# Optimization experiments

Hardware: AMD Instinct MI355X
Metric: run time of the kernel (lower is better)

Reference implementation:

```python
import jax, jax.numpy as jnp
import numpy as np

B, N, H, W = 8, 16384, 64, 64
CTX, OUT, ST = 32, 2, 1
HID = [516, 256, 128, 64, 32, 16]
IN_SIZE = CTX + 2 + ST + OUT  # 37


def _bilinear_sample(img, coord):
    """torch F.grid_sample, mode=bilinear, padding=zeros, align_corners=False.
    img: [B,C,H,W]; coord: [B,N,2] (x,y in [-1,1]). Returns [B,C,N]."""
    _, _, Hh, Ww = img.shape
    gx = (coord[..., 0] + 1.0) * (Ww * 0.5) - 0.5
    gy = (coord[..., 1] + 1.0) * (Hh * 0.5) - 0.5
    x0 = jnp.floor(gx)
    y0 = jnp.floor(gy)
    wx1 = gx - x0
    wy1 = gy - y0

    def tap(xi, yi, w):
        valid = (xi >= 0) & (xi < Ww) & (yi >= 0) & (yi < Hh)
        xc = jnp.clip(xi, 0, Ww - 1).astype(jnp.int32)
        yc = jnp.clip(yi, 0, Hh - 1).astype(jnp.int32)
        vals = jax.vmap(lambda im, y, x: im[:, y, x])(img, yc, xc)  # [B,C,N]
        return vals * (w * valid)[:, None, :]

    return (tap(x0, y0, (1 - wx1) * (1 - wy1))
            + tap(x0 + 1, y0, wx1 * (1 - wy1))
            + tap(x0, y0 + 1, (1 - wx1) * wy1)
            + tap(x0 + 1, y0 + 1, wx1 * wy1))


def _layer_shapes():
    shapes = [(IN_SIZE, HID[0])]
    for i in range(len(HID) - 1):
        shapes.append((HID[i] + IN_SIZE, HID[i + 1]))
    shapes.append((HID[-1], OUT))
    return shapes


def setup_inputs():
    key = jax.random.key(0)
    ks = jax.random.split(key, 4 + 7)
    inp = {
        "lr_fields": jax.random.normal(ks[0], (B, OUT, H, W), jnp.float32),
        "context_grid": jax.random.normal(ks[1], (B, CTX, H, W), jnp.float32),
        "hr_eps": jax.random.normal(ks[2], (B, H, W), jnp.float32),
        "coord": jax.random.uniform(ks[3], (B, N, 2), jnp.float32, -1.0, 1.0),
    }
    for j, (fi, fo) in enumerate(_layer_shapes()):
        inp[f"W{j}"] = jax.random.normal(ks[4 + j], (fi, fo), jnp.float32) / np.sqrt(fi)
        inp[f"b{j}"] = jnp.zeros((fo,), jnp.float32)
    return inp


def reference(lr_fields, context_grid, hr_eps, coord,
              W0, b0, W1, b1, W2, b2, W3, b3, W4, b4, W5, b5, W6, b6):
    # original permutes (0,1,3,2) before grid_sample -> swap spatial axes
    ctx_pts = _bilinear_sample(jnp.swapaxes(context_grid, 2, 3), coord)  # [B,CTX,N]
    lr_pts = _bilinear_sample(jnp.swapaxes(lr_fields, 2, 3), coord)      # [B,OUT,N]
    eps_pts = _bilinear_sample(jnp.swapaxes(hr_eps[:, None], 2, 3), coord)  # [B,1,N]
    x_in = jnp.concatenate([
        jnp.transpose(ctx_pts, (0, 2, 1)),
        coord,
        jnp.transpose(lr_pts, (0, 2, 1)),
        jnp.transpose(eps_pts, (0, 2, 1)),
    ], axis=2)  # [B,N,37]
    x = jax.nn.relu(x_in @ W0 + b0)
    for Wl, bl in ((W1, b1), (W2, b2), (W3, b3), (W4, b4), (W5, b5)):
        x = jax.nn.relu(jnp.concatenate([x, x_in], axis=2) @ Wl + bl)
    return x @ W6 + b6  # [B,N,2]
```

## Files before the change

kernel.cpp:

```cpp
#include <hip/hip_runtime.h>


#define NTH     1024
#define NWAVES  16
#define MPTS    32
#define MTILES  (MPTS / 16)
#define SROW    872
#define XIN_OFF 0
#define HA_OFF  64
#define HB_OFF  608
#define NPOINTS (8 * 16384)
#define GRIDX   (NPOINTS / MPTS)
#define LDSBYTES (MPTS * SROW * 2)

#define SGB __builtin_amdgcn_sched_group_barrier
#define SG_MFMA   0x008
#define SG_VMREAD 0x020
#define SG_DSREAD 0x100

typedef short          short8  __attribute__((ext_vector_type(8)));
typedef short          short4v __attribute__((ext_vector_type(4)));
typedef float          f32x4   __attribute__((ext_vector_type(4)));
typedef unsigned short u16;

__device__ __forceinline__ u16 f2bf(float f) {
    unsigned int u = __builtin_bit_cast(unsigned int, f);
    u += 0x7fffu + ((u >> 16) & 1u);
    return (u16)(u >> 16);
}

__constant__ int pk_base8[8] = {0, 4224, 23680, 28800, 30336, 30848, 31040, 31104};
__constant__ int pk_ks[7]    = {2, 19, 10, 6, 4, 3, 1};
__constant__ int pk_khp[7]   = {0, 544, 256, 128, 64, 32, 32};
__constant__ int pk_kact[7]  = {0, 516, 256, 128, 64, 32, 16};
__constant__ int pk_nact[7]  = {516, 256, 128, 64, 32, 16, 2};

struct WPtrs { const float* W[7]; };

__global__ void pack_weights(WPtrs wp, u16* __restrict__ out)
{
    const int f = blockIdx.x * blockDim.x + threadIdx.x;
    if (f >= 31104) return;
    int l = 0;
    while (l < 6 && f >= pk_base8[l + 1]) ++l;
    const int r    = f - pk_base8[l];
    const int lane = r & 63;
    const int t    = r >> 6;
    const int ks   = pk_ks[l];
    const int s    = t % ks;
    const int nt   = t / ks;
    const int n    = nt * 16 + (lane & 15);
    const int k0   = s * 32 + (lane >> 4) * 8;
    const int nact = pk_nact[l];
    const int khp  = pk_khp[l];
    const int kact = pk_kact[l];
    const float* W = wp.W[l];

    union { short8 v; u16 e[8]; } frag;
#pragma unroll
    for (int j = 0; j < 8; ++j) {
        const int k = k0 + j;
        float v = 0.0f;
        if (n < nact) {
            if (k < khp) {
                if (k < kact) v = W[k * nact + n];
            } else {
                const int xr = k - khp;
                if (xr < 37) v = W[(kact + xr) * nact + n];
            }
        }
        frag.e[j] = f2bf(v);
    }
    *(short8*)(out + (size_t)f * 8) = frag.v;
}

template<int KHP, int HSEG, int OSEG, int NT, int NACT, int LBASE,
         bool XIN, bool RELU, bool GOUT>
__device__ __forceinline__ void mlayer(const u16* __restrict__ wpack,
                                       const float* __restrict__ bias,
                                       u16* __restrict__ s_act,
                                       float* __restrict__ gout, int p0,
                                       int wave, int lane)
{
    constexpr int KHS = KHP / 32;
    constexpr int KS  = KHS + (XIN ? 2 : 0);
    constexpr int MS  = MTILES;
    const int lm = lane & 15;
    const int lq = lane >> 4;
    const u16* wl = wpack + LBASE + lane * 8;

    const u16* arow[MS];
#pragma unroll
    for (int m = 0; m < MS; ++m)
        arow[m] = s_act + (m * 16 + lm) * SROW + lq * 8;

    for (int nt = wave; nt < NT; nt += NWAVES) {
        const u16* bp = wl + (size_t)nt * KS * 512;

        f32x4 acc[MS];
#pragma unroll
        for (int m = 0; m < MS; ++m)
            acc[m] = (f32x4){0.f, 0.f, 0.f, 0.f};

#pragma unroll
        for (int s = 0; s < KS; ++s) {
            const int ab = (s < KHS) ? (HSEG + s * 32)
                                     : (XIN_OFF + (s - KHS) * 32);
            short8 a[MS];
#pragma unroll
            for (int m = 0; m < MS; ++m)
                a[m] = *(const short8*)(arow[m] + ab);
            const short8 b = *(const short8*)(bp + (size_t)s * 512);
#pragma unroll
            for (int m = 0; m < MS; ++m)
                acc[m] = __builtin_amdgcn_mfma_f32_16x16x32_bf16(b, a[m], acc[m], 0, 0, 0);
        }

        SGB(SG_DSREAD, 2, 0); SGB(SG_VMREAD, 1, 0);
        if (KS > 1) { SGB(SG_DSREAD, 2, 0); SGB(SG_VMREAD, 1, 0); }
#pragma unroll
        for (int s = 0; s < KS; ++s) {
            SGB(SG_MFMA, 2, 0);
            if (s + 2 < KS) { SGB(SG_DSREAD, 2, 0); SGB(SG_VMREAD, 1, 0); }
        }

        const int bn = nt * 16 + lq * 4;
        float bv[4];
        if (bn + 4 <= NACT) {
            const f32x4 b4 = *(const f32x4*)(bias + bn);
            bv[0] = b4[0]; bv[1] = b4[1]; bv[2] = b4[2]; bv[3] = b4[3];
        } else {
#pragma unroll
            for (int r = 0; r < 4; ++r)
                bv[r] = (bn + r < NACT) ? bias[bn + r] : 0.f;
        }
        if (GOUT) {
            if (lq == 0) {
#pragma unroll
                for (int m = 0; m < MS; ++m) {
                    float2 o;
                    o.x = acc[m][0] + bv[0];
                    o.y = acc[m][1] + bv[1];
                    *(float2*)(gout + (size_t)(p0 + m * 16 + lm) * 2) = o;
                }
            }
        } else {
#pragma unroll
            for (int m = 0; m < MS; ++m) {
                short4v o;
#pragma unroll
                for (int r = 0; r < 4; ++r) {
                    float v = acc[m][r] + bv[r];
                    if (RELU) v = fmaxf(v, 0.f);
                    o[r] = (short)f2bf(v);
                }
                *(short4v*)(s_act + (size_t)(m * 16 + lm) * SROW + OSEG + bn) = o;
            }
        }
    }
}

struct MainParams {
    const float* lr;
    const float* ctx;
    const float* eps;
    const float* coord;
    const float* Bb[7];
    const u16*   wpack;
    float*       out;
};

__global__ __launch_bounds__(NTH, 8)
void cont_decoder_mfma(MainParams p)
{
    extern __shared__ u16 s_act[];
    __shared__ int   s_x0[MPTS], s_y0[MPTS];
    __shared__ float s_wx[MPTS], s_wy[MPTS];

    const int tid  = threadIdx.x;
    const int wave = tid >> 6;
    const int lane = tid & 63;
    const int p0   = blockIdx.x * MPTS;
    const int b    = p0 >> 14;

    for (int i = tid; i < MPTS * 43; i += NTH) {
        const int pt = i / 43, c = i % 43;
        const int col = (c < 27) ? (37 + c) : (592 + (c - 27));
        s_act[pt * SROW + col] = 0;
    }

    if (tid < MPTS) {
        const int pt = p0 + tid;
        const float cx = p.coord[2 * pt];
        const float cy = p.coord[2 * pt + 1];
        const float gx = (cx + 1.0f) * 32.0f - 0.5f;
        const float gy = (cy + 1.0f) * 32.0f - 0.5f;
        const float fx0 = floorf(gx), fy0 = floorf(gy);
        s_x0[tid] = (int)fx0;
        s_y0[tid] = (int)fy0;
        s_wx[tid] = gx - fx0;
        s_wy[tid] = gy - fy0;
        s_act[tid * SROW + 32] = f2bf(cx);
        s_act[tid * SROW + 33] = f2bf(cy);
    }
    __syncthreads();

    for (int idx = tid; idx < MPTS * 35; idx += NTH) {
        const int t = idx / 35;
        const int c = idx % 35;
        const float* base;
        int col;
        if (c < 32)      { base = p.ctx + (size_t)(b * 32 + c) * 4096;       col = c; }
        else if (c < 34) { base = p.lr  + (size_t)(b * 2 + (c - 32)) * 4096; col = 34 + (c - 32); }
        else             { base = p.eps + (size_t)b * 4096;                   col = 36; }

        const int   x0 = s_x0[t], y0 = s_y0[t];
        const float wx = s_wx[t], wy = s_wy[t];
        const int x1 = x0 + 1, y1 = y0 + 1;
        const bool xv0 = (x0 >= 0) & (x0 < 64);
        const bool xv1 = (x1 >= 0) & (x1 < 64);
        const bool yv0 = (y0 >= 0) & (y0 < 64);
        const bool yv1 = (y1 >= 0) & (y1 < 64);
        const int xc0 = min(max(x0, 0), 63), xc1 = min(max(x1, 0), 63);
        const int yc0 = min(max(y0, 0), 63), yc1 = min(max(y1, 0), 63);

        const float w00 = (1.0f - wx) * (1.0f - wy) * ((xv0 && yv0) ? 1.0f : 0.0f);
        const float w10 = wx * (1.0f - wy)          * ((xv1 && yv0) ? 1.0f : 0.0f);
        const float w01 = (1.0f - wx) * wy          * ((xv0 && yv1) ? 1.0f : 0.0f);
        const float w11 = wx * wy                   * ((xv1 && yv1) ? 1.0f : 0.0f);

        const float val = w00 * base[xc0 * 64 + yc0]
                        + w10 * base[xc1 * 64 + yc0]
                        + w01 * base[xc0 * 64 + yc1]
                        + w11 * base[xc1 * 64 + yc1];
        s_act[t * SROW + col] = f2bf(val);
    }
    __syncthreads();

    mlayer<  0,  HA_OFF, HA_OFF, 33, 516, 0,      true,  true,  false>(p.wpack, p.Bb[0], s_act, nullptr, p0, wave, lane);
    __syncthreads();
    mlayer<544,  HA_OFF, HB_OFF, 16, 256, 33792,  true,  true,  false>(p.wpack, p.Bb[1], s_act, nullptr, p0, wave, lane);
    __syncthreads();
    mlayer<256,  HB_OFF, HA_OFF,  8, 128, 189440, true,  true,  false>(p.wpack, p.Bb[2], s_act, nullptr, p0, wave, lane);
    __syncthreads();
    mlayer<128,  HA_OFF, HB_OFF,  4,  64, 230400, true,  true,  false>(p.wpack, p.Bb[3], s_act, nullptr, p0, wave, lane);
    __syncthreads();
    mlayer< 64,  HB_OFF, HA_OFF,  2,  32, 242688, true,  true,  false>(p.wpack, p.Bb[4], s_act, nullptr, p0, wave, lane);
    __syncthreads();
    mlayer< 32,  HA_OFF, HB_OFF,  1,  16, 246784, true,  true,  false>(p.wpack, p.Bb[5], s_act, nullptr, p0, wave, lane);
    __syncthreads();
    mlayer< 32,  HB_OFF, 0,       1,   2, 248320, false, false, true >(p.wpack, p.Bb[6], s_act, p.out,   p0, wave, lane);
}

extern "C" void kernel_launch(void* const* d_in, const int* in_sizes, int n_in,
                              void* d_out, int out_size, void* d_ws, size_t ws_size,
                              hipStream_t stream)
{
    WPtrs wp;
    for (int l = 0; l < 7; ++l) wp.W[l] = (const float*)d_in[4 + 2 * l];

    MainParams p;
    p.lr    = (const float*)d_in[0];
    p.ctx   = (const float*)d_in[1];
    p.eps   = (const float*)d_in[2];
    p.coord = (const float*)d_in[3];
    for (int l = 0; l < 7; ++l) p.Bb[l] = (const float*)d_in[5 + 2 * l];
    p.wpack = (const u16*)d_ws;
    p.out   = (float*)d_out;

    hipFuncSetAttribute((const void*)cont_decoder_mfma,
                        hipFuncAttributeMaxDynamicSharedMemorySize, LDSBYTES);

    hipLaunchKernelGGL(pack_weights, dim3(122), dim3(256), 0, stream, wp, (u16*)d_ws);
    hipLaunchKernelGGL(cont_decoder_mfma, dim3(GRIDX), dim3(NTH), LDSBYTES, stream, p);
}
```

Measured before the change: 220.8 us.

## Hand-pipeline MFMA operand loads with inline asm rings and explicit waitcnts

Replaces compiler-scheduled LDS and global operand loads in the MLP layer loop with inline-asm ds_read_b128 and global_load_dwordx4 issued into small ring buffers. Activations are prefetched three k-steps ahead and weights two ahead, with explicit s_waitcnt counters before each MFMA step. The goal is to overlap load latency with MFMA work more predictably than the sched_group_barrier hints did. In exchange it adds register pressure under 1024-thread launch bounds. The hand-counted waitcnts are fragile, since any compiler-generated memory operation in between would break the counts.

```diff
diff --git a/kernel.cpp b/kernel.cpp
--- a/kernel.cpp
+++ b/kernel.cpp
@@ -13,11 +13,6 @@
 #define GRIDX   (NPOINTS / MPTS)
 #define LDSBYTES (MPTS * SROW * 2)
 
-#define SGB __builtin_amdgcn_sched_group_barrier
-#define SG_MFMA   0x008
-#define SG_VMREAD 0x020
-#define SG_DSREAD 0x100
-
 typedef short          short8  __attribute__((ext_vector_type(8)));
 typedef short          short4v __attribute__((ext_vector_type(4)));
 typedef float          f32x4   __attribute__((ext_vector_type(4)));
@@ -28,6 +23,28 @@
     u += 0x7fffu + ((u >> 16) & 1u);
     return (u16)(u >> 16);
 }
+
+__device__ __forceinline__ unsigned lds_off(const void* p) {
+    return (unsigned)(unsigned long long)
+        (__attribute__((address_space(3))) const void*)p;
+}
+
+__device__ __forceinline__ short8 dsread128(unsigned addr) {
+    short8 d;
+    asm volatile("ds_read_b128 %0, %1" : "=v"(d) : "v"(addr));
+    return d;
+}
+__device__ __forceinline__ short8 gload128(const void* p) {
+    short8 d;
+    asm volatile("global_load_dwordx4 %0, %1, off" : "=v"(d) : "v"(p));
+    return d;
+}
+
+__device__ __forceinline__ void wvm0(){ asm volatile("s_waitcnt vmcnt(0)"   ::: "memory"); }
+__device__ __forceinline__ void wvm1(){ asm volatile("s_waitcnt vmcnt(1)"   ::: "memory"); }
+__device__ __forceinline__ void wlg0(){ asm volatile("s_waitcnt lgkmcnt(0)" ::: "memory"); }
+__device__ __forceinline__ void wlg2(){ asm volatile("s_waitcnt lgkmcnt(2)" ::: "memory"); }
+__device__ __forceinline__ void wlg4(){ asm volatile("s_waitcnt lgkmcnt(4)" ::: "memory"); }
 
 __constant__ int pk_base8[8] = {0, 4224, 23680, 28800, 30336, 30848, 31040, 31104};
 __constant__ int pk_ks[7]    = {2, 19, 10, 6, 4, 3, 1};
@@ -84,15 +101,19 @@
 {
     constexpr int KHS = KHP / 32;
     constexpr int KS  = KHS + (XIN ? 2 : 0);
+    constexpr int DA  = (KS < 3) ? KS : 3;
+    constexpr int DW  = (KS < 2) ? KS : 2;
     constexpr int MS  = MTILES;
     const int lm = lane & 15;
     const int lq = lane >> 4;
     const u16* wl = wpack + LBASE + lane * 8;
 
-    const u16* arow[MS];
+#define ABOFF(s_) (((s_) < KHS) ? (HSEG + (s_) * 32) : (XIN_OFF + ((s_) - KHS) * 32))
+
+    unsigned abase[MS];
 #pragma unroll
     for (int m = 0; m < MS; ++m)
-        arow[m] = s_act + (m * 16 + lm) * SROW + lq * 8;
+        abase[m] = lds_off(s_act + ((m * 16 + lm) * SROW + lq * 8));
 
     for (int nt = wave; nt < NT; nt += NWAVES) {
         const u16* bp = wl + (size_t)nt * KS * 512;
@@ -102,26 +123,37 @@
         for (int m = 0; m < MS; ++m)
             acc[m] = (f32x4){0.f, 0.f, 0.f, 0.f};
 
+        wlg0(); wvm0();
+
+        short8 wring[DW];
+#pragma unroll
+        for (int d = 0; d < DW; ++d)
+            wring[d] = gload128(bp + (size_t)d * 512);
+        short8 aring[DA][MS];
+#pragma unroll
+        for (int d = 0; d < DA; ++d)
+#pragma unroll
+            for (int m = 0; m < MS; ++m)
+                aring[d][m] = dsread128(abase[m] + 2u * ABOFF(d));
+
 #pragma unroll
         for (int s = 0; s < KS; ++s) {
-            const int ab = (s < KHS) ? (HSEG + s * 32)
-                                     : (XIN_OFF + (s - KHS) * 32);
-            short8 a[MS];
+            const int wv = ((KS - s) < DW ? (KS - s) : DW) - 1;
+            if (wv >= 1) wvm1(); else wvm0();
+            const int la = ((KS - s) < DA ? (KS - s) : DA) - 1;
+            if (la >= 2) wlg4(); else if (la == 1) wlg2(); else wlg0();
+            __builtin_amdgcn_sched_barrier(0);
 #pragma unroll
             for (int m = 0; m < MS; ++m)
-                a[m] = *(const short8*)(arow[m] + ab);
-            const short8 b = *(const short8*)(bp + (size_t)s * 512);
-#pragma unroll
-            for (int m = 0; m < MS; ++m)
-                acc[m] = __builtin_amdgcn_mfma_f32_16x16x32_bf16(b, a[m], acc[m], 0, 0, 0);
-        }
-
-        SGB(SG_DSREAD, 2, 0); SGB(SG_VMREAD, 1, 0);
-        if (KS > 1) { SGB(SG_DSREAD, 2, 0); SGB(SG_VMREAD, 1, 0); }
-#pragma unroll
-        for (int s = 0; s < KS; ++s) {
-            SGB(SG_MFMA, 2, 0);
-            if (s + 2 < KS) { SGB(SG_DSREAD, 2, 0); SGB(SG_VMREAD, 1, 0); }
+                acc[m] = __builtin_amdgcn_mfma_f32_16x16x32_bf16(
+                             wring[s % DW], aring[s % DA][m], acc[m], 0, 0, 0);
+            if (s + DW < KS)
+                wring[s % DW] = gload128(bp + (size_t)(s + DW) * 512);
+            if (s + DA < KS) {
+#pragma unroll
+                for (int m = 0; m < MS; ++m)
+                    aring[s % DA][m] = dsread128(abase[m] + 2u * ABOFF(s + DA));
+            }
         }
 
         const int bn = nt * 16 + lq * 4;
@@ -158,6 +190,7 @@
             }
         }
     }
+#undef ABOFF
 }
 
 struct MainParams {
```

Result: no change. 218.4 us (-1.1%).

## Double points per block and compute hidden layers in place with one LDS buffer

Applied to the files above, without the earlier changes.

Doubles the points handled per block from 32 to 64, so each weight fragment loaded from global memory feeds twice as many MFMAs. Replaces the two ping-pong activation buffers with a single in-place hidden segment: each wave keeps its accumulators in registers across a barrier, then overwrites the shared buffer, shrinking the row stride. This trades less global weight traffic for more registers per wave and an extra barrier per layer, and it drops the manual sched_group_barrier instruction interleaving. The first layer still loops over 33 column tiles, but writing them in place is safe because its only inputs are the x_in columns.

```diff
diff --git a/kernel.cpp b/kernel.cpp
--- a/kernel.cpp
+++ b/kernel.cpp
@@ -3,20 +3,14 @@
 
 #define NTH     1024
 #define NWAVES  16
-#define MPTS    32
+#define MPTS    64
 #define MTILES  (MPTS / 16)
-#define SROW    872
+#define SROW    616
 #define XIN_OFF 0
-#define HA_OFF  64
-#define HB_OFF  608
+#define HSEG    64
 #define NPOINTS (8 * 16384)
 #define GRIDX   (NPOINTS / MPTS)
 #define LDSBYTES (MPTS * SROW * 2)
-
-#define SGB __builtin_amdgcn_sched_group_barrier
-#define SG_MFMA   0x008
-#define SG_VMREAD 0x020
-#define SG_DSREAD 0x100
 
 typedef short          short8  __attribute__((ext_vector_type(8)));
 typedef short          short4v __attribute__((ext_vector_type(4)));
@@ -74,89 +68,54 @@
     *(short8*)(out + (size_t)f * 8) = frag.v;
 }
 
-template<int KHP, int HSEG, int OSEG, int NT, int NACT, int LBASE,
-         bool XIN, bool RELU, bool GOUT>
-__device__ __forceinline__ void mlayer(const u16* __restrict__ wpack,
-                                       const float* __restrict__ bias,
-                                       u16* __restrict__ s_act,
-                                       float* __restrict__ gout, int p0,
-                                       int wave, int lane)
+template<int KHP, bool XIN, int MS>
+__device__ __forceinline__ void unit_compute(const u16* __restrict__ bp,
+                                             const u16* const* arow,
+                                             f32x4* acc)
 {
     constexpr int KHS = KHP / 32;
     constexpr int KS  = KHS + (XIN ? 2 : 0);
-    constexpr int MS  = MTILES;
-    const int lm = lane & 15;
-    const int lq = lane >> 4;
-    const u16* wl = wpack + LBASE + lane * 8;
-
-    const u16* arow[MS];
-#pragma unroll
-    for (int m = 0; m < MS; ++m)
-        arow[m] = s_act + (m * 16 + lm) * SROW + lq * 8;
-
-    for (int nt = wave; nt < NT; nt += NWAVES) {
-        const u16* bp = wl + (size_t)nt * KS * 512;
-
-        f32x4 acc[MS];
+#pragma unroll
+    for (int s = 0; s < KS; ++s) {
+        const int ab = (s < KHS) ? (HSEG + s * 32)
+                                 : (XIN_OFF + (s - KHS) * 32);
+        short8 a[MS];
 #pragma unroll
         for (int m = 0; m < MS; ++m)
-            acc[m] = (f32x4){0.f, 0.f, 0.f, 0.f};
-
-#pragma unroll
-        for (int s = 0; s < KS; ++s) {
-            const int ab = (s < KHS) ? (HSEG + s * 32)
-                                     : (XIN_OFF + (s - KHS) * 32);
-            short8 a[MS];
-#pragma unroll
-            for (int m = 0; m < MS; ++m)
-                a[m] = *(const short8*)(arow[m] + ab);
-            const short8 b = *(const short8*)(bp + (size_t)s * 512);
-#pragma unroll
-            for (int m = 0; m < MS; ++m)
-                acc[m] = __builtin_amdgcn_mfma_f32_16x16x32_bf16(b, a[m], acc[m], 0, 0, 0);
-        }
-
-        SGB(SG_DSREAD, 2, 0); SGB(SG_VMREAD, 1, 0);
-        if (KS > 1) { SGB(SG_DSREAD, 2, 0); SGB(SG_VMREAD, 1, 0); }
-#pragma unroll
-        for (int s = 0; s < KS; ++s) {
-            SGB(SG_MFMA, 2, 0);
-            if (s + 2 < KS) { SGB(SG_DSREAD, 2, 0); SGB(SG_VMREAD, 1, 0); }
-        }
-
-        const int bn = nt * 16 + lq * 4;
-        float bv[4];
-        if (bn + 4 <= NACT) {
-            const f32x4 b4 = *(const f32x4*)(bias + bn);
-            bv[0] = b4[0]; bv[1] = b4[1]; bv[2] = b4[2]; bv[3] = b4[3];
-        } else {
-#pragma unroll
-            for (int r = 0; r < 4; ++r)
-                bv[r] = (bn + r < NACT) ? bias[bn + r] : 0.f;
-        }
-        if (GOUT) {
-            if (lq == 0) {
-#pragma unroll
-                for (int m = 0; m < MS; ++m) {
-                    float2 o;
-                    o.x = acc[m][0] + bv[0];
-                    o.y = acc[m][1] + bv[1];
-                    *(float2*)(gout + (size_t)(p0 + m * 16 + lm) * 2) = o;
-                }
-            }
-        } else {
-#pragma unroll
-            for (int m = 0; m < MS; ++m) {
-                short4v o;
-#pragma unroll
-                for (int r = 0; r < 4; ++r) {
-                    float v = acc[m][r] + bv[r];
-                    if (RELU) v = fmaxf(v, 0.f);
-                    o[r] = (short)f2bf(v);
-                }
-                *(short4v*)(s_act + (size_t)(m * 16 + lm) * SROW + OSEG + bn) = o;
-            }
-        }
+            a[m] = *(const short8*)(arow[m] + ab);
+        const short8 b = *(const short8*)(bp + (size_t)s * 512);
+#pragma unroll
+        for (int m = 0; m < MS; ++m)
+            acc[m] = __builtin_amdgcn_mfma_f32_16x16x32_bf16(b, a[m], acc[m], 0, 0, 0);
+    }
+}
+
+template<int NACT, bool RELU, int MS>
+__device__ __forceinline__ void unit_store_lds(const f32x4* acc,
+                                               const float* __restrict__ bias,
+                                               u16* __restrict__ s_act,
+                                               int nt, int lm, int lq)
+{
+    const int bn = nt * 16 + lq * 4;
+    float bv[4];
+    if (bn + 4 <= NACT) {
+        const f32x4 b4 = *(const f32x4*)(bias + bn);
+        bv[0] = b4[0]; bv[1] = b4[1]; bv[2] = b4[2]; bv[3] = b4[3];
+    } else {
+#pragma unroll
+        for (int r = 0; r < 4; ++r)
+            bv[r] = (bn + r < NACT) ? bias[bn + r] : 0.f;
+    }
+#pragma unroll
+    for (int m = 0; m < MS; ++m) {
+        short4v o;
+#pragma unroll
+        for (int r = 0; r < 4; ++r) {
+            float v = acc[m][r] + bv[r];
+            if (RELU) v = fmaxf(v, 0.f);
+            o[r] = (short)f2bf(v);
+        }
+        *(short4v*)(s_act + (size_t)(m * 16 + lm) * SROW + HSEG + bn) = o;
     }
 }
 
@@ -170,6 +129,30 @@
     float*       out;
 };
 
+template<int KHP, int NT, int NACT, int LBASE>
+__device__ __forceinline__ void mlayer_ip(const u16* __restrict__ wpack,
+                                          const float* __restrict__ bias,
+                                          u16* __restrict__ s_act,
+                                          const u16* const* arow,
+                                          int wave, int lane)
+{
+    constexpr int MS = MTILES;
+    const int lm = lane & 15;
+    const int lq = lane >> 4;
+    f32x4 acc[MS];
+#pragma unroll
+    for (int m = 0; m < MS; ++m) acc[m] = (f32x4){0.f, 0.f, 0.f, 0.f};
+
+    const bool active = (wave < NT);
+    if (active) {
+        const u16* bp = wpack + LBASE + lane * 8 + (size_t)wave * (KHP / 32 + 2) * 512;
+        unit_compute<KHP, true, MS>(bp, arow, acc);
+    }
+    __syncthreads();
+    if (active)
+        unit_store_lds<NACT, true, MS>(acc, bias, s_act, wave, lm, lq);
+}
+
 __global__ __launch_bounds__(NTH, 8)
 void cont_decoder_mfma(MainParams p)
 {
@@ -180,6 +163,8 @@
     const int tid  = threadIdx.x;
     const int wave = tid >> 6;
     const int lane = tid & 63;
+    const int lm   = lane & 15;
+    const int lq   = lane >> 4;
     const int p0   = blockIdx.x * MPTS;
     const int b    = p0 >> 14;
 
@@ -237,19 +222,51 @@
     }
     __syncthreads();
 
-    mlayer<  0,  HA_OFF, HA_OFF, 33, 516, 0,      true,  true,  false>(p.wpack, p.Bb[0], s_act, nullptr, p0, wave, lane);
-    __syncthreads();
-    mlayer<544,  HA_OFF, HB_OFF, 16, 256, 33792,  true,  true,  false>(p.wpack, p.Bb[1], s_act, nullptr, p0, wave, lane);
-    __syncthreads();
-    mlayer<256,  HB_OFF, HA_OFF,  8, 128, 189440, true,  true,  false>(p.wpack, p.Bb[2], s_act, nullptr, p0, wave, lane);
-    __syncthreads();
-    mlayer<128,  HA_OFF, HB_OFF,  4,  64, 230400, true,  true,  false>(p.wpack, p.Bb[3], s_act, nullptr, p0, wave, lane);
-    __syncthreads();
-    mlayer< 64,  HB_OFF, HA_OFF,  2,  32, 242688, true,  true,  false>(p.wpack, p.Bb[4], s_act, nullptr, p0, wave, lane);
-    __syncthreads();
-    mlayer< 32,  HA_OFF, HB_OFF,  1,  16, 246784, true,  true,  false>(p.wpack, p.Bb[5], s_act, nullptr, p0, wave, lane);
-    __syncthreads();
-    mlayer< 32,  HB_OFF, 0,       1,   2, 248320, false, false, true >(p.wpack, p.Bb[6], s_act, p.out,   p0, wave, lane);
+    const u16* arow[MTILES];
+#pragma unroll
+    for (int m = 0; m < MTILES; ++m)
+        arow[m] = s_act + (m * 16 + lm) * SROW + lq * 8;
+
+    {
+        for (int nt = wave; nt < 33; nt += NWAVES) {
+            f32x4 acc[MTILES];
+#pragma unroll
+            for (int m = 0; m < MTILES; ++m) acc[m] = (f32x4){0.f, 0.f, 0.f, 0.f};
+            const u16* bp = p.wpack + 0 + lane * 8 + (size_t)nt * 2 * 512;
+            unit_compute<0, true, MTILES>(bp, arow, acc);
+            unit_store_lds<516, true, MTILES>(acc, p.Bb[0], s_act, nt, lm, lq);
+        }
+    }
+    __syncthreads();
+
+    mlayer_ip<544, 16, 256, 33792 >(p.wpack, p.Bb[1], s_act, arow, wave, lane);
+    __syncthreads();
+    mlayer_ip<256,  8, 128, 189440>(p.wpack, p.Bb[2], s_act, arow, wave, lane);
+    __syncthreads();
+    mlayer_ip<128,  4,  64, 230400>(p.wpack, p.Bb[3], s_act, arow, wave, lane);
+    __syncthreads();
+    mlayer_ip< 64,  2,  32, 242688>(p.wpack, p.Bb[4], s_act, arow, wave, lane);
+    __syncthreads();
+    mlayer_ip< 32,  1,  16, 246784>(p.wpack, p.Bb[5], s_act, arow, wave, lane);
+    __syncthreads();
+
+    if (wave == 0) {
+        f32x4 acc[MTILES];
+#pragma unroll
+        for (int m = 0; m < MTILES; ++m) acc[m] = (f32x4){0.f, 0.f, 0.f, 0.f};
+        const u16* bp = p.wpack + 248320 + lane * 8;
+        unit_compute<32, false, MTILES>(bp, arow, acc);
+        if (lq == 0) {
+            const float b0 = p.Bb[6][0], b1 = p.Bb[6][1];
+#pragma unroll
+            for (int m = 0; m < MTILES; ++m) {
+                float2 o;
+                o.x = acc[m][0] + b0;
+                o.y = acc[m][1] + b1;
+                *(float2*)(p.out + (size_t)(p0 + m * 16 + lm) * 2) = o;
+            }
+        }
+    }
 }
 
 extern "C" void kernel_launch(void* const* d_in, const int* in_sizes, int n_in,
```

After: 222.2 us. No clear change (+0.6%).

## Double points per block, 2x8 wave grid, in-place activations with barrier

Applied to the files above, without the earlier changes.

Raises points per block from 32 to 64 and splits the 16 waves into 2 M-groups by 8 N-groups, each wave computing a 2x2 block of MFMA tiles so every loaded weight fragment is reused across more points. Activation ping-pong buffers are merged into one in-place hidden segment, with an internal __syncthreads between the compute and store phases for layers that read and write the same region. This shrinks the LDS row stride and halves grid size and per-point weight traffic, at the cost of more LDS per block, fewer blocks, and removal of the explicit scheduling barriers. Layer 0 reads only the input region, so it writes in place without the extra barrier.

```diff
diff --git a/kernel.cpp b/kernel.cpp
--- a/kernel.cpp
+++ b/kernel.cpp
@@ -3,20 +3,14 @@
 
 #define NTH     1024
 #define NWAVES  16
-#define MPTS    32
+#define MPTS    64
 #define MTILES  (MPTS / 16)
-#define SROW    872
+#define SROW    616
 #define XIN_OFF 0
-#define HA_OFF  64
-#define HB_OFF  608
+#define HSEG    64
 #define NPOINTS (8 * 16384)
 #define GRIDX   (NPOINTS / MPTS)
 #define LDSBYTES (MPTS * SROW * 2)
-
-#define SGB __builtin_amdgcn_sched_group_barrier
-#define SG_MFMA   0x008
-#define SG_VMREAD 0x020
-#define SG_DSREAD 0x100
 
 typedef short          short8  __attribute__((ext_vector_type(8)));
 typedef short          short4v __attribute__((ext_vector_type(4)));
@@ -74,92 +68,6 @@
     *(short8*)(out + (size_t)f * 8) = frag.v;
 }
 
-template<int KHP, int HSEG, int OSEG, int NT, int NACT, int LBASE,
-         bool XIN, bool RELU, bool GOUT>
-__device__ __forceinline__ void mlayer(const u16* __restrict__ wpack,
-                                       const float* __restrict__ bias,
-                                       u16* __restrict__ s_act,
-                                       float* __restrict__ gout, int p0,
-                                       int wave, int lane)
-{
-    constexpr int KHS = KHP / 32;
-    constexpr int KS  = KHS + (XIN ? 2 : 0);
-    constexpr int MS  = MTILES;
-    const int lm = lane & 15;
-    const int lq = lane >> 4;
-    const u16* wl = wpack + LBASE + lane * 8;
-
-    const u16* arow[MS];
-#pragma unroll
-    for (int m = 0; m < MS; ++m)
-        arow[m] = s_act + (m * 16 + lm) * SROW + lq * 8;
-
-    for (int nt = wave; nt < NT; nt += NWAVES) {
-        const u16* bp = wl + (size_t)nt * KS * 512;
-
-        f32x4 acc[MS];
-#pragma unroll
-        for (int m = 0; m < MS; ++m)
-            acc[m] = (f32x4){0.f, 0.f, 0.f, 0.f};
-
-#pragma unroll
-        for (int s = 0; s < KS; ++s) {
-            const int ab = (s < KHS) ? (HSEG + s * 32)
-                                     : (XIN_OFF + (s - KHS) * 32);
-            short8 a[MS];
-#pragma unroll
-            for (int m = 0; m < MS; ++m)
-                a[m] = *(const short8*)(arow[m] + ab);
-            const short8 b = *(const short8*)(bp + (size_t)s * 512);
-#pragma unroll
-            for (int m = 0; m < MS; ++m)
-                acc[m] = __builtin_amdgcn_mfma_f32_16x16x32_bf16(b, a[m], acc[m], 0, 0, 0);
-        }
-
-        SGB(SG_DSREAD, 2, 0); SGB(SG_VMREAD, 1, 0);
-        if (KS > 1) { SGB(SG_DSREAD, 2, 0); SGB(SG_VMREAD, 1, 0); }
-#pragma unroll
-        for (int s = 0; s < KS; ++s) {
-            SGB(SG_MFMA, 2, 0);
-            if (s + 2 < KS) { SGB(SG_DSREAD, 2, 0); SGB(SG_VMREAD, 1, 0); }
-        }
-
-        const int bn = nt * 16 + lq * 4;
-        float bv[4];
-        if (bn + 4 <= NACT) {
-            const f32x4 b4 = *(const f32x4*)(bias + bn);
-            bv[0] = b4[0]; bv[1] = b4[1]; bv[2] = b4[2]; bv[3] = b4[3];
-        } else {
-#pragma unroll
-            for (int r = 0; r < 4; ++r)
-                bv[r] = (bn + r < NACT) ? bias[bn + r] : 0.f;
-        }
-        if (GOUT) {
-            if (lq == 0) {
-#pragma unroll
-                for (int m = 0; m < MS; ++m) {
-                    float2 o;
-                    o.x = acc[m][0] + bv[0];
-                    o.y = acc[m][1] + bv[1];
-                    *(float2*)(gout + (size_t)(p0 + m * 16 + lm) * 2) = o;
-                }
-            }
-        } else {
-#pragma unroll
-            for (int m = 0; m < MS; ++m) {
-                short4v o;
-#pragma unroll
-                for (int r = 0; r < 4; ++r) {
-                    float v = acc[m][r] + bv[r];
-                    if (RELU) v = fmaxf(v, 0.f);
-                    o[r] = (short)f2bf(v);
-                }
-                *(short4v*)(s_act + (size_t)(m * 16 + lm) * SROW + OSEG + bn) = o;
-            }
-        }
-    }
-}
-
 struct MainParams {
     const float* lr;
     const float* ctx;
@@ -169,6 +77,140 @@
     const u16*   wpack;
     float*       out;
 };
+
+template<int NACT, bool RELU>
+__device__ __forceinline__ void store_nt(const f32x4* accm,
+                                         const float* __restrict__ bias,
+                                         u16* __restrict__ s_act,
+                                         int nt, int mbase, int lm, int lq)
+{
+    const int bn = nt * 16 + lq * 4;
+    float bv[4];
+    if (bn + 4 <= NACT) {
+        const f32x4 b4 = *(const f32x4*)(bias + bn);
+        bv[0] = b4[0]; bv[1] = b4[1]; bv[2] = b4[2]; bv[3] = b4[3];
+    } else {
+#pragma unroll
+        for (int r = 0; r < 4; ++r)
+            bv[r] = (bn + r < NACT) ? bias[bn + r] : 0.f;
+    }
+#pragma unroll
+    for (int m = 0; m < 2; ++m) {
+        short4v o;
+#pragma unroll
+        for (int r = 0; r < 4; ++r) {
+            float v = accm[m][r] + bv[r];
+            if (RELU) v = fmaxf(v, 0.f);
+            o[r] = (short)f2bf(v);
+        }
+        *(short4v*)(s_act + (size_t)((mbase + m) * 16 + lm) * SROW + HSEG + bn) = o;
+    }
+}
+
+template<int KHP, int NT, int NACT, int LBASE,
+         bool XIN, bool RELU, bool GOUT, bool IPBAR>
+__device__ __forceinline__ void mlayer(const u16* __restrict__ wpack,
+                                       const float* __restrict__ bias,
+                                       u16* __restrict__ s_act,
+                                       float* __restrict__ gout, int p0,
+                                       int wave, int lane)
+{
+    constexpr int KHS = KHP / 32;
+    constexpr int KS  = KHS + (XIN ? 2 : 0);
+    const int lm = lane & 15;
+    const int lq = lane >> 4;
+    const int mg = wave & 1;
+    const int ng = wave >> 1;
+    const int mbase = mg * 2;
+
+    const u16* arow0 = s_act + (size_t)((mbase * 16) + lm) * SROW + lq * 8;
+    const u16* arow1 = arow0 + (size_t)16 * SROW;
+    const u16* wl = wpack + LBASE + lane * 8;
+
+#define ABOFF(s_) (((s_) < KHS) ? (HSEG + (s_) * 32) : (XIN_OFF + ((s_) - KHS) * 32))
+
+    if constexpr (IPBAR) {
+        const int nt0 = ng, nt1 = ng + 8;
+        const bool act0 = nt0 < NT;
+        const bool act1 = nt1 < NT;
+        f32x4 acc[2][2];
+#pragma unroll
+        for (int i = 0; i < 2; ++i)
+#pragma unroll
+            for (int m = 0; m < 2; ++m)
+                acc[i][m] = (f32x4){0.f, 0.f, 0.f, 0.f};
+
+        if (act0) {
+            const u16* bp0 = wl + (size_t)nt0 * KS * 512;
+            const u16* bp1 = wl + (size_t)nt1 * KS * 512;
+#pragma unroll
+            for (int s = 0; s < KS; ++s) {
+                const int ab = ABOFF(s);
+                const short8 a0 = *(const short8*)(arow0 + ab);
+                const short8 a1 = *(const short8*)(arow1 + ab);
+                const short8 w0 = *(const short8*)(bp0 + (size_t)s * 512);
+                acc[0][0] = __builtin_amdgcn_mfma_f32_16x16x32_bf16(w0, a0, acc[0][0], 0, 0, 0);
+                acc[0][1] = __builtin_amdgcn_mfma_f32_16x16x32_bf16(w0, a1, acc[0][1], 0, 0, 0);
+                if (act1) {
+                    const short8 w1 = *(const short8*)(bp1 + (size_t)s * 512);
+                    acc[1][0] = __builtin_amdgcn_mfma_f32_16x16x32_bf16(w1, a0, acc[1][0], 0, 0, 0);
+                    acc[1][1] = __builtin_amdgcn_mfma_f32_16x16x32_bf16(w1, a1, acc[1][1], 0, 0, 0);
+                }
+            }
+        }
+        __syncthreads();
+        if (act0) store_nt<NACT, RELU>(acc[0], bias, s_act, nt0, mbase, lm, lq);
+        if (act1) store_nt<NACT, RELU>(acc[1], bias, s_act, nt1, mbase, lm, lq);
+    } else {
+        for (int g = 0;; ++g) {
+            const int nt0 = ng + 16 * g;
+            if (nt0 >= NT) break;
+            const int nt1 = nt0 + 8;
+            const bool act1 = nt1 < NT;
+            f32x4 acc[2][2];
+#pragma unroll
+            for (int i = 0; i < 2; ++i)
+#pragma unroll
+                for (int m = 0; m < 2; ++m)
+                    acc[i][m] = (f32x4){0.f, 0.f, 0.f, 0.f};
+
+            const u16* bp0 = wl + (size_t)nt0 * KS * 512;
+            const u16* bp1 = wl + (size_t)nt1 * KS * 512;
+#pragma unroll
+            for (int s = 0; s < KS; ++s) {
+                const int ab = ABOFF(s);
+                const short8 a0 = *(const short8*)(arow0 + ab);
+                const short8 a1 = *(const short8*)(arow1 + ab);
+                const short8 w0 = *(const short8*)(bp0 + (size_t)s * 512);
+                acc[0][0] = __builtin_amdgcn_mfma_f32_16x16x32_bf16(w0, a0, acc[0][0], 0, 0, 0);
+                acc[0][1] = __builtin_amdgcn_mfma_f32_16x16x32_bf16(w0, a1, acc[0][1], 0, 0, 0);
+                if (act1) {
+                    const short8 w1 = *(const short8*)(bp1 + (size_t)s * 512);
+                    acc[1][0] = __builtin_amdgcn_mfma_f32_16x16x32_bf16(w1, a0, acc[1][0], 0, 0, 0);
+                    acc[1][1] = __builtin_amdgcn_mfma_f32_16x16x32_bf16(w1, a1, acc[1][1], 0, 0, 0);
+                }
+            }
+
+            if (GOUT) {
+                if (lq == 0) {
+                    const float b0 = bias[0], b1 = bias[1];
+#pragma unroll
+                    for (int m = 0; m < 2; ++m) {
+                        float2 o;
+                        o.x = acc[0][m][0] + b0;
+                        o.y = acc[0][m][1] + b1;
+                        *(float2*)(gout + (size_t)(p0 + (mbase + m) * 16 + lm) * 2) = o;
+                    }
+                }
+            } else {
+                store_nt<NACT, RELU>(acc[0], bias, s_act, nt0, mbase, lm, lq);
+                if (act1)
+                    store_nt<NACT, RELU>(acc[1], bias, s_act, nt1, mbase, lm, lq);
+            }
+        }
+    }
+#undef ABOFF
+}
 
 __global__ __launch_bounds__(NTH, 8)
 void cont_decoder_mfma(MainParams p)
@@ -237,19 +279,19 @@
     }
     __syncthreads();
 
-    mlayer<  0,  HA_OFF, HA_OFF, 33, 516, 0,      true,  true,  false>(p.wpack, p.Bb[0], s_act, nullptr, p0, wave, lane);
-    __syncthreads();
-    mlayer<544,  HA_OFF, HB_OFF, 16, 256, 33792,  true,  true,  false>(p.wpack, p.Bb[1], s_act, nullptr, p0, wave, lane);
-    __syncthreads();
-    mlayer<256,  HB_OFF, HA_OFF,  8, 128, 189440, true,  true,  false>(p.wpack, p.Bb[2], s_act, nullptr, p0, wave, lane);
-    __syncthreads();
-    mlayer<128,  HA_OFF, HB_OFF,  4,  64, 230400, true,  true,  false>(p.wpack, p.Bb[3], s_act, nullptr, p0, wave, lane);
-    __syncthreads();
-    mlayer< 64,  HB_OFF, HA_OFF,  2,  32, 242688, true,  true,  false>(p.wpack, p.Bb[4], s_act, nullptr, p0, wave, lane);
-    __syncthreads();
-    mlayer< 32,  HA_OFF, HB_OFF,  1,  16, 246784, true,  true,  false>(p.wpack, p.Bb[5], s_act, nullptr, p0, wave, lane);
-    __syncthreads();
-    mlayer< 32,  HB_OFF, 0,       1,   2, 248320, false, false, true >(p.wpack, p.Bb[6], s_act, p.out,   p0, wave, lane);
+    mlayer<  0, 33, 516, 0,      true,  true,  false, false>(p.wpack, p.Bb[0], s_act, nullptr, p0, wave, lane);
+    __syncthreads();
+    mlayer<544, 16, 256, 33792,  true,  true,  false, true >(p.wpack, p.Bb[1], s_act, nullptr, p0, wave, lane);
+    __syncthreads();
+    mlayer<256,  8, 128, 189440, true,  true,  false, true >(p.wpack, p.Bb[2], s_act, nullptr, p0, wave, lane);
+    __syncthreads();
+    mlayer<128,  4,  64, 230400, true,  true,  false, true >(p.wpack, p.Bb[3], s_act, nullptr, p0, wave, lane);
+    __syncthreads();
+    mlayer< 64,  2,  32, 242688, true,  true,  false, true >(p.wpack, p.Bb[4], s_act, nullptr, p0, wave, lane);
+    __syncthreads();
+    mlayer< 32,  1,  16, 246784, true,  true,  false, true >(p.wpack, p.Bb[5], s_act, nullptr, p0, wave, lane);
+    __syncthreads();
+    mlayer< 32,  1,   2, 248320, false, false, true,  false>(p.wpack, p.Bb[6], s_act, p.out,   p0, wave, lane);
 }
 
 extern "C" void kernel_launch(void* const* d_in, const int* in_sizes, int n_in,
```

Result: faster. 211.2 us (-4.4%).
